# Performance work log

Measured on AMD Instinct MI355X. Metric: run time of the kernel, lower is better.

## Reference

```python
import jax, jax.numpy as jnp
import numpy as np

N = 8192      # total QM atoms (concatenated over batch)
L = 6         # num_interactions / trajectory length
F = 256       # hidden_size
FH = F // 2
D_RBF = 32    # distance_embedding_size
E = 131072    # total probe edges
P = 32768     # total probes
CUTOFF = 4.0


def silu(x):
    return x * jax.nn.sigmoid(x)


def setup_inputs() -> dict:
    key = jax.random.key(0)
    ks = jax.random.split(key, 20)
    g = lambda k, shp, s=1.0: jax.random.normal(k, shp, dtype=jnp.float32) * s
    s_stack = g(ks[0], (N, L, F))
    v_stack = g(ks[1], (N, L, 3, F))
    # positions in a 2A box so all probe-atom distances < cutoff=4A
    atom_xyz = jax.random.uniform(ks[2], (N, 3), dtype=jnp.float32) * 2.0
    probe_xyz = jax.random.uniform(ks[3], (P, 3), dtype=jnp.float32) * 2.0
    cell = jnp.eye(3, dtype=jnp.float32) * 2.0
    probe_edges_displacement = jnp.zeros((E, 3), dtype=jnp.float32)
    atom_idx = jax.random.randint(ks[4], (E,), 0, N)
    probe_idx = jax.random.randint(ks[5], (E,), 0, P)
    probe_edges = jnp.stack([atom_idx, probe_idx], axis=1)
    in_dim = D_RBF + 3 * F  # e_pi || q_pi || n_i || S_JK
    return {
        's_stack': s_stack,
        'v_stack': v_stack,
        'atom_xyz': atom_xyz,
        'probe_xyz': probe_xyz,
        'cell': cell,
        'probe_edges_displacement': probe_edges_displacement,
        # JK attention MLP: F -> F/2 -> 1
        'attn_w1': g(ks[6], (F, FH), 1.0 / np.sqrt(F)),
        'attn_b1': jnp.zeros((FH,), jnp.float32),
        'attn_w2': g(ks[7], (FH, 1), 1.0 / np.sqrt(FH)),
        'attn_b2': jnp.zeros((1,), jnp.float32),
        # readout msg MLP: (D_rbf+3F) -> F -> F/2 -> 1
        'msg_w1': g(ks[8], (in_dim, F), 1.0 / np.sqrt(in_dim)),
        'msg_b1': jnp.zeros((F,), jnp.float32),
        'msg_w2': g(ks[9], (F, FH), 1.0 / np.sqrt(F)),
        'msg_b2': jnp.zeros((FH,), jnp.float32),
        'msg_w3': g(ks[10], (FH, 1), 1.0 / np.sqrt(FH)),
        'msg_b3': jnp.zeros((1,), jnp.float32),
        'probe_edges': probe_edges,
    }


def reference(s_stack, v_stack, atom_xyz, probe_xyz, cell, probe_edges_displacement,
              attn_w1, attn_b1, attn_w2, attn_b2,
              msg_w1, msg_b1, msg_w2, msg_b2, msg_w3, msg_b3,
              probe_edges):
    # ---- JKNetAggregation: node-level attention over layer trajectory ----
    h = silu(jnp.einsum('nlf,fh->nlh', s_stack, attn_w1) + attn_b1)   # [N,L,F/2]
    logits = (jnp.einsum('nlh,ho->nlo', h, attn_w2) + attn_b2)[..., 0]  # [N,L]
    a = jax.nn.softmax(logits, axis=1)                                  # [N,L]
    S_JK = jnp.einsum('nl,nlf->nf', a, s_stack)                         # [N,F]
    V_JK = jnp.einsum('nl,nlcf->ncf', a, v_stack)                       # [N,3,F]

    # ---- InfoBottleneckReadout: gather -> per-edge MLP -> scatter ----
    atom_idx = probe_edges[:, 0]
    probe_idx = probe_edges[:, 1]
    shift = probe_edges_displacement @ cell                             # [E,3] PBC shift
    diff = probe_xyz[probe_idx] - (atom_xyz[atom_idx] + shift)          # [E,3]
    dist = jnp.linalg.norm(diff, axis=-1)                               # [E]
    d = dist[:, None]
    n = jnp.arange(1, D_RBF + 1, dtype=jnp.float32)
    e_pi = jnp.sin(d * n * jnp.pi / CUTOFF) / (d + 1e-8)                # [E,D_rbf] sinc RBF
    r_hat = diff / (d + 1e-8)                                           # [E,3]
    V_e = V_JK[atom_idx]                                                # [E,3,F]
    q_pi = jnp.einsum('ecf,ec->ef', V_e, r_hat)                         # [E,F]
    n_i = jnp.linalg.norm(V_JK, axis=1)                                 # [N,F]
    h_pi = jnp.concatenate([e_pi, q_pi, n_i[atom_idx], S_JK[atom_idx]], axis=-1)  # [E,D_rbf+3F]
    m = silu(h_pi @ msg_w1 + msg_b1)
    m = silu(m @ msg_w2 + msg_b2)
    m = (m @ msg_w3 + msg_b3)[:, 0]                                     # [E]
    cw = jnp.where(dist < CUTOFF, 0.5 * (jnp.cos(jnp.pi * dist / CUTOFF) + 1.0), 0.0)
    rho = jax.ops.segment_sum(m * cw, probe_idx, num_segments=P)        # [P]
    return rho
```

## Files before the change

### kernel.cpp

```cpp
#include <hip/hip_runtime.h>
#include <math.h>
#include <stdint.h>


#define L_DIM 6
#define F_DIM 256
#define FH_DIM 128
#define DRBF 32
#define CUTOFF_F 4.0f
#define PI_F 3.14159265358979323846f

using bf16x8 = __attribute__((ext_vector_type(8))) short;
using f32x4v = __attribute__((ext_vector_type(4))) float;

__device__ __forceinline__ float silu_f(float x){ return x / (1.f + __expf(-x)); }

__device__ __forceinline__ unsigned short f2bf(float f){
    uint32_t u = __float_as_uint(f);
    uint32_t r = (u + 0x7fffu + ((u >> 16) & 1u)) >> 16;
    return (unsigned short)r;
}

__global__ __launch_bounds__(256) void kPrep(
    const float* __restrict__ msg_w1, const float* __restrict__ msg_w2,
    const float* __restrict__ attn_w1,
    unsigned short* __restrict__ w1bt, unsigned short* __restrict__ w1cdt,
    unsigned short* __restrict__ w2t, unsigned short* __restrict__ wA1t,
    float* __restrict__ rho, int P, int* __restrict__ cntpos, int CN)
{
    int idx = blockIdx.x * 256 + threadIdx.x;
    if (idx < 65536){
        int k = idx >> 8, j = idx & 255;
        w1bt[(size_t)j * 256 + k] = f2bf(msg_w1[(size_t)(DRBF + k) * F_DIM + j]);
    } else if (idx < 196608){
        int i2 = idx - 65536;
        int k = i2 >> 8, j = i2 & 255;
        w1cdt[(size_t)j * 512 + k] = f2bf(msg_w1[(size_t)(DRBF + 256 + k) * F_DIM + j]);
    } else if (idx < 229376){
        int i3 = idx - 196608;
        int k = i3 >> 7, h = i3 & 127;
        w2t[(size_t)h * 256 + k] = f2bf(msg_w2[(size_t)k * FH_DIM + h]);
    } else if (idx < 262144){
        int i4 = idx - 229376;
        int j = i4 >> 8, k = i4 & 255;
        wA1t[(size_t)j * 256 + k] = f2bf(attn_w1[(size_t)k * FH_DIM + j]);
    } else if (idx < 262144 + 32768){
        int i5 = idx - 262144;
        if (i5 < P) rho[i5] = 0.f;
    } else {
        int i6 = idx - 262144 - 32768;
        if (i6 < CN) cntpos[i6] = 0;
    }
}

__global__ __launch_bounds__(256) void kAW(
    const float* __restrict__ s_stack, const float* __restrict__ v_stack,
    const unsigned short* __restrict__ wA1t,
    const float* __restrict__ attn_b1, const float* __restrict__ attn_w2,
    unsigned short* __restrict__ VJKb, unsigned short* __restrict__ NISb, int N)
{
    __shared__ float part[4][48];
    __shared__ float aw_l[8][8];

    const int t  = threadIdx.x;
    const int l  = t & 63;
    const int w  = t >> 6;
    const int lm = l & 15, lq = l >> 4;

    bf16x8 bfr[2][8];
    #pragma unroll
    for (int nt2 = 0; nt2 < 2; nt2++){
        const int col = w*32 + nt2*16 + lm;
        #pragma unroll
        for (int kb = 0; kb < 8; kb++)
            bfr[nt2][kb] = *(const bf16x8*)(wA1t + (size_t)col * 256 + kb*32 + lq*8);
    }
    const float b1a = attn_b1[w*32 + lm];
    const float b1b = attn_b1[w*32 + 16 + lm];
    const float w2a = attn_w2[w*32 + lm];
    const float w2b = attn_w2[w*32 + 16 + lm];

    const int n0 = blockIdx.x * 8;
    const size_t rbase = (size_t)n0 * L_DIM;
    const size_t rmax  = (size_t)N * L_DIM - 1;

    #pragma unroll
    for (int mt = 0; mt < 3; mt++){
        const size_t r0 = rbase + mt * 16;
        bf16x8 af[8];
        #pragma unroll
        for (int kb = 0; kb < 8; kb++){
            size_t row = r0 + lm; if (row > rmax) row = rmax;
            const float* ap = s_stack + row * 256 + kb*32 + lq*8;
            float4 fa = *(const float4*)ap;
            float4 fb = *(const float4*)(ap + 4);
            bf16x8 v;
            v[0] = (short)f2bf(fa.x); v[1] = (short)f2bf(fa.y);
            v[2] = (short)f2bf(fa.z); v[3] = (short)f2bf(fa.w);
            v[4] = (short)f2bf(fb.x); v[5] = (short)f2bf(fb.y);
            v[6] = (short)f2bf(fb.z); v[7] = (short)f2bf(fb.w);
            af[kb] = v;
        }
        f32x4v a0 = {0.f,0.f,0.f,0.f}, a1 = {0.f,0.f,0.f,0.f};
        #pragma unroll
        for (int kb = 0; kb < 8; kb++){
            a0 = __builtin_amdgcn_mfma_f32_16x16x32_bf16(af[kb], bfr[0][kb], a0, 0, 0, 0);
            a1 = __builtin_amdgcn_mfma_f32_16x16x32_bf16(af[kb], bfr[1][kb], a1, 0, 0, 0);
        }
        #pragma unroll
        for (int r = 0; r < 4; r++){
            float p = silu_f(a0[r] + b1a) * w2a + silu_f(a1[r] + b1b) * w2b;
            #pragma unroll
            for (int m = 8; m >= 1; m >>= 1) p += __shfl_xor(p, m, 64);
            if (lm == 0) part[w][mt*16 + lq*4 + r] = p;
        }
    }
    __syncthreads();
    if (t < 48) part[0][t] = part[0][t] + part[1][t] + part[2][t] + part[3][t];
    __syncthreads();
    if (t < 8){
        float e[L_DIM]; float mx = -1e30f;
        #pragma unroll
        for (int l6 = 0; l6 < L_DIM; l6++) mx = fmaxf(mx, part[0][t*L_DIM + l6]);
        float s = 0.f;
        #pragma unroll
        for (int l6 = 0; l6 < L_DIM; l6++){ e[l6] = __expf(part[0][t*L_DIM + l6] - mx); s += e[l6]; }
        float inv = 1.f / s;
        #pragma unroll
        for (int l6 = 0; l6 < L_DIM; l6++) aw_l[t][l6] = e[l6] * inv;
    }
    __syncthreads();

    #pragma unroll
    for (int aa = 0; aa < 2; aa++){
        const int n = min(n0 + w*2 + aa, N - 1);
        float aw[L_DIM];
        #pragma unroll
        for (int l6 = 0; l6 < L_DIM; l6++) aw[l6] = aw_l[w*2 + aa][l6];

        const float* sp = s_stack + (size_t)n * (L_DIM * F_DIM) + l * 4;
        const float* vp = v_stack + (size_t)n * (L_DIM * 3 * F_DIM) + l * 4;
        float4 v0 = {0.f,0.f,0.f,0.f}, v1 = {0.f,0.f,0.f,0.f}, v2 = {0.f,0.f,0.f,0.f};
        float4 sj = {0.f,0.f,0.f,0.f};
        #pragma unroll
        for (int l6 = 0; l6 < L_DIM; l6++){
            const float a = aw[l6];
            float4 ss = *(const float4*)(sp + (size_t)l6 * F_DIM);
            float4 x0 = *(const float4*)(vp + (size_t)(l6*3+0) * F_DIM);
            float4 x1 = *(const float4*)(vp + (size_t)(l6*3+1) * F_DIM);
            float4 x2 = *(const float4*)(vp + (size_t)(l6*3+2) * F_DIM);
            v0.x = fmaf(a, x0.x, v0.x); v0.y = fmaf(a, x0.y, v0.y);
            v0.z = fmaf(a, x0.z, v0.z); v0.w = fmaf(a, x0.w, v0.w);
            v1.x = fmaf(a, x1.x, v1.x); v1.y = fmaf(a, x1.y, v1.y);
            v1.z = fmaf(a, x1.z, v1.z); v1.w = fmaf(a, x1.w, v1.w);
            v2.x = fmaf(a, x2.x, v2.x); v2.y = fmaf(a, x2.y, v2.y);
            v2.z = fmaf(a, x2.z, v2.z); v2.w = fmaf(a, x2.w, v2.w);
            sj.x = fmaf(a, ss.x, sj.x); sj.y = fmaf(a, ss.y, sj.y);
            sj.z = fmaf(a, ss.z, sj.z); sj.w = fmaf(a, ss.w, sj.w);
        }
        float4 ni;
        ni.x = sqrtf(v0.x*v0.x + v1.x*v1.x + v2.x*v2.x);
        ni.y = sqrtf(v0.y*v0.y + v1.y*v1.y + v2.y*v2.y);
        ni.z = sqrtf(v0.z*v0.z + v1.z*v1.z + v2.z*v2.z);
        ni.w = sqrtf(v0.w*v0.w + v1.w*v1.w + v2.w*v2.w);

        ushort4 o;
        o = (ushort4){f2bf(v0.x), f2bf(v0.y), f2bf(v0.z), f2bf(v0.w)};
        *(ushort4*)&VJKb[((size_t)n*3 + 0) * F_DIM + l*4] = o;
        o = (ushort4){f2bf(v1.x), f2bf(v1.y), f2bf(v1.z), f2bf(v1.w)};
        *(ushort4*)&VJKb[((size_t)n*3 + 1) * F_DIM + l*4] = o;
        o = (ushort4){f2bf(v2.x), f2bf(v2.y), f2bf(v2.z), f2bf(v2.w)};
        *(ushort4*)&VJKb[((size_t)n*3 + 2) * F_DIM + l*4] = o;
        o = (ushort4){f2bf(ni.x), f2bf(ni.y), f2bf(ni.z), f2bf(ni.w)};
        *(ushort4*)&NISb[(size_t)n * 512 + l*4] = o;
        o = (ushort4){f2bf(sj.x), f2bf(sj.y), f2bf(sj.z), f2bf(sj.w)};
        *(ushort4*)&NISb[(size_t)n * 512 + 256 + l*4] = o;
    }
}

__global__ __launch_bounds__(256) void kA2(
    const unsigned short* __restrict__ VJKb, const unsigned short* __restrict__ w1bt,
    const unsigned short* __restrict__ NISb, const unsigned short* __restrict__ w1cdt,
    const float* __restrict__ msg_b1,
    float* __restrict__ UT4, int gU)
{
    const int t  = threadIdx.x;
    const int l  = t & 63;
    const int w  = t >> 6;
    const int lm = l & 15, lq = l >> 4;

    if ((int)blockIdx.x < gU){
        bf16x8 bfr[4][8];
        #pragma unroll
        for (int ct = 0; ct < 4; ct++)
            #pragma unroll
            for (int kb = 0; kb < 8; kb++)
                bfr[ct][kb] = *(const bf16x8*)(w1bt + (size_t)(w*64 + ct*16 + lm) * 256 + kb*32 + lq*8);

        const int r00 = blockIdx.x * 128;
        #pragma unroll 1
        for (int mt = 0; mt < 8; mt++){
            const int r0 = r00 + mt * 16;
            bf16x8 af[8];
            #pragma unroll
            for (int kb = 0; kb < 8; kb++)
                af[kb] = *(const bf16x8*)(VJKb + (size_t)(r0 + lm) * 256 + kb*32 + lq*8);
            f32x4v acc[4];
            #pragma unroll
            for (int ct = 0; ct < 4; ct++) acc[ct] = (f32x4v){0.f,0.f,0.f,0.f};
            #pragma unroll
            for (int kb = 0; kb < 8; kb++)
                #pragma unroll
                for (int ct = 0; ct < 4; ct++)
                    acc[ct] = __builtin_amdgcn_mfma_f32_16x16x32_bf16(af[kb], bfr[ct][kb], acc[ct], 0, 0, 0);
            #pragma unroll
            for (int ct = 0; ct < 4; ct++){
                const int col = w*64 + ct*16 + lm;
                #pragma unroll
                for (int r = 0; r < 4; r++){
                    const int row = r0 + lq*4 + r;
                    const int n = row / 3, c = row - n*3;
                    UT4[(((size_t)n << 8) + col) * 4 + c] = acc[ct][r];
                }
            }
        }
    } else {
        const int bid = blockIdx.x - gU;
        const int ch = bid & 1;
        const int bm = bid >> 1;

        bf16x8 bfr[2][16];
        #pragma unroll
        for (int ct = 0; ct < 2; ct++)
            #pragma unroll
            for (int kb = 0; kb < 16; kb++)
                bfr[ct][kb] = *(const bf16x8*)(w1cdt + (size_t)(ch*128 + w*32 + ct*16 + lm) * 512 + kb*32 + lq*8);

        const int r00 = bm * 128;
        #pragma unroll 1
        for (int mt = 0; mt < 8; mt++){
            const int r0 = r00 + mt * 16;
            bf16x8 af[16];
            #pragma unroll
            for (int kb = 0; kb < 16; kb++)
                af[kb] = *(const bf16x8*)(NISb + (size_t)(r0 + lm) * 512 + kb*32 + lq*8);
            f32x4v acc[2];
            #pragma unroll
            for (int ct = 0; ct < 2; ct++) acc[ct] = (f32x4v){0.f,0.f,0.f,0.f};
            #pragma unroll
            for (int kb = 0; kb < 16; kb++)
                #pragma unroll
                for (int ct = 0; ct < 2; ct++)
                    acc[ct] = __builtin_amdgcn_mfma_f32_16x16x32_bf16(af[kb], bfr[ct][kb], acc[ct], 0, 0, 0);
            #pragma unroll
            for (int ct = 0; ct < 2; ct++){
                const int col = ch*128 + w*32 + ct*16 + lm;
                const float bias = msg_b1[col];
                #pragma unroll
                for (int r = 0; r < 4; r++){
                    const int n = r0 + lq*4 + r;
                    UT4[(((size_t)n << 8) + col) * 4 + 3] = acc[ct][r] + bias;
                }
            }
        }
    }
}

__global__ __launch_bounds__(256) void kHist(const int* __restrict__ pe, int* __restrict__ cnt, int E){
    int e = blockIdx.x * 256 + threadIdx.x;
    if (e < E) atomicAdd(&cnt[pe[(size_t)e*2]], 1);
}

__global__ __launch_bounds__(1024) void kScan(const int* __restrict__ cnt, int* __restrict__ off, int N){
    __shared__ int sums[1024];
    const int t = threadIdx.x;
    const int base = t * 8;
    int c[8]; int s = 0;
    #pragma unroll
    for (int j = 0; j < 8; j++){
        int v = (base + j < N) ? cnt[base + j] : 0;
        c[j] = s; s += v;
    }
    sums[t] = s;
    __syncthreads();
    for (int d = 1; d < 1024; d <<= 1){
        int v = (t >= d) ? sums[t - d] : 0;
        __syncthreads();
        sums[t] += v;
        __syncthreads();
    }
    int excl = (t == 0) ? 0 : sums[t - 1];
    #pragma unroll
    for (int j = 0; j < 8; j++)
        if (base + j < N) off[base + j] = excl + c[j];
    if (t == 1023) off[N] = sums[1023];
}

__global__ __launch_bounds__(256) void kScatter(const int* __restrict__ pe,
    const int* __restrict__ off, int* __restrict__ pos, int* __restrict__ perm, int E){
    int e = blockIdx.x * 256 + threadIdx.x;
    if (e < E){
        int i = pe[(size_t)e*2];
        int slot = atomicAdd(&pos[i], 1);
        perm[off[i] + slot] = e;
    }
}

__global__ __launch_bounds__(256) void kB1(
    const int* __restrict__ pe, const float* __restrict__ disp,
    const float* __restrict__ cell,
    const float* __restrict__ atom_xyz, const float* __restrict__ probe_xyz,
    const float* __restrict__ UT4,
    const float* __restrict__ msg_w1,
    const unsigned short* __restrict__ w2t, const float* __restrict__ msg_b2,
    const float* __restrict__ msg_w3, const float* __restrict__ msg_b3,
    const int* __restrict__ perm,
    float* __restrict__ rho, int E)
{
    __shared__ unsigned short x_lds[32 * 256];
    __shared__ unsigned short epi_b[32 * 40];
    __shared__ int   ai_l[32];
    __shared__ int   pp_l[32];
    __shared__ float4 rc4_l[32];
    __shared__ float part[4][32];

    char* xbase = (char*)x_lds;

    const int t  = threadIdx.x;
    const int l  = t & 63;
    const int w  = t >> 6;
    const int lq = l >> 4;
    const int lm = l & 15;

    const float c0 = cell[0], c1 = cell[1], c2 = cell[2];
    const float c3 = cell[3], c4 = cell[4], c5 = cell[5];
    const float c6 = cell[6], c7 = cell[7], c8 = cell[8];

    bf16x8 w1afr[4];
    #pragma unroll
    for (int nt = 0; nt < 4; nt++){
        const int col = w*64 + nt*16 + lm;
        bf16x8 v;
        #pragma unroll
        for (int j = 0; j < 8; j++)
            v[j] = (short)f2bf(msg_w1[(size_t)(lq*8 + j) * F_DIM + col]);
        w1afr[nt] = v;
    }

    bf16x8 bfr[2][8];
    #pragma unroll
    for (int nt2 = 0; nt2 < 2; nt2++){
        const int h = w*32 + nt2*16 + lm;
        #pragma unroll
        for (int kb = 0; kb < 8; kb++)
            bfr[nt2][kb] = *(const bf16x8*)(w2t + (size_t)h * F_DIM + kb*32 + lq*8);
    }
    const float b2v0 = msg_b2[w*32 + lm];
    const float b2v1 = msg_b2[w*32 + 16 + lm];
    const float w3v0 = msg_w3[w*32 + lm];
    const float w3v1 = msg_w3[w*32 + 16 + lm];
    const float b3   = msg_b3[0];

    const int e0 = blockIdx.x * 128;

    int ee_r[4], ia_r[4], ip_r[4];
    #pragma unroll
    for (int bb = 0; bb < 4; bb++){
        int s = min(e0 + bb*32 + (t >> 3), E - 1);
        ee_r[bb] = perm[s];
    }
    #pragma unroll
    for (int bb = 0; bb < 4; bb++){
        ia_r[bb] = pe[(size_t)ee_r[bb]*2];
        ip_r[bb] = pe[(size_t)ee_r[bb]*2 + 1];
    }

    #pragma unroll 1
    for (int bb = 0; bb < 4; bb++){
        const int e0b = e0 + bb * 32;

        {
            const int slot = t >> 3, q = t & 7;
            const int ee = ee_r[bb];
            const int ia = ia_r[bb];
            const int ip = ip_r[bb];
            const float d0 = disp[(size_t)ee*3], d1 = disp[(size_t)ee*3+1], d2 = disp[(size_t)ee*3+2];
            const float sx = d0*c0 + d1*c3 + d2*c6;
            const float sy = d0*c1 + d1*c4 + d2*c7;
            const float sz = d0*c2 + d1*c5 + d2*c8;
            const float dx = probe_xyz[(size_t)ip*3+0] - (atom_xyz[(size_t)ia*3+0] + sx);
            const float dy = probe_xyz[(size_t)ip*3+1] - (atom_xyz[(size_t)ia*3+1] + sy);
            const float dz = probe_xyz[(size_t)ip*3+2] - (atom_xyz[(size_t)ia*3+2] + sz);
            const float dist = sqrtf(dx*dx + dy*dy + dz*dz);
            const float inv  = 1.f / (dist + 1e-8f);
            const float base = dist * (PI_F / CUTOFF_F);
            ushort4 eb;
            eb.x = f2bf(__sinf(base * (float)(q*4 + 1)) * inv);
            eb.y = f2bf(__sinf(base * (float)(q*4 + 2)) * inv);
            eb.z = f2bf(__sinf(base * (float)(q*4 + 3)) * inv);
            eb.w = f2bf(__sinf(base * (float)(q*4 + 4)) * inv);
            *(ushort4*)&epi_b[slot*40 + q*4] = eb;
            if (q == 0){
                ai_l[slot] = ia;
                pp_l[slot] = ip;
                float cw = (dist < CUTOFF_F) ? 0.5f * (__cosf(base) + 1.f) : 0.f;
                rc4_l[slot] = (float4){dx*inv, dy*inv, dz*inv, cw};
            }
        }
        __syncthreads();

        f32x4v pacc[2][4];
        #pragma unroll
        for (int mt = 0; mt < 2; mt++)
            #pragma unroll
            for (int nt = 0; nt < 4; nt++) pacc[mt][nt] = (f32x4v){0.f,0.f,0.f,0.f};
        #pragma unroll
        for (int mt = 0; mt < 2; mt++){
            const bf16x8 af = *(const bf16x8*)&epi_b[(mt*16 + lm)*40 + lq*8];
            #pragma unroll
            for (int nt = 0; nt < 4; nt++)
                pacc[mt][nt] = __builtin_amdgcn_mfma_f32_16x16x32_bf16(af, w1afr[nt], pacc[mt][nt], 0, 0, 0);
        }

        #pragma unroll
        for (int mt = 0; mt < 2; mt++){
            #pragma unroll
            for (int r = 0; r < 4; r++){
                const int e = mt*16 + lq*4 + r;
                const int i = ai_l[e];
                const float4 rc = rc4_l[e];
                const float* up = UT4 + ((size_t)i << 10);
                #pragma unroll
                for (int nt = 0; nt < 4; nt++){
                    const int col = w*64 + nt*16 + lm;
                    const float4 ut = *(const float4*)(up + (size_t)col * 4);
                    float z = pacc[mt][nt][r] + ut.w;
                    z = fmaf(rc.x, ut.x, fmaf(rc.y, ut.y, fmaf(rc.z, ut.z, z)));
                    const int wofs = e*512 + ((col*2) ^ ((e & 7) << 4));
                    *(unsigned short*)(xbase + wofs) = f2bf(silu_f(z));
                }
            }
        }
        __syncthreads();

        f32x4v acc00 = {0.f,0.f,0.f,0.f}, acc01 = {0.f,0.f,0.f,0.f};
        f32x4v acc10 = {0.f,0.f,0.f,0.f}, acc11 = {0.f,0.f,0.f,0.f};
        const int eA0 = lm;
        const int eA1 = 16 + lm;
        #pragma unroll
        for (int kb = 0; kb < 8; kb++){
            const int ko = kb*64 + lq*16;
            bf16x8 af0 = *(const bf16x8*)(xbase + eA0*512 + (ko ^ ((eA0 & 7) << 4)));
            bf16x8 af1 = *(const bf16x8*)(xbase + eA1*512 + (ko ^ ((eA1 & 7) << 4)));
            acc00 = __builtin_amdgcn_mfma_f32_16x16x32_bf16(af0, bfr[0][kb], acc00, 0, 0, 0);
            acc01 = __builtin_amdgcn_mfma_f32_16x16x32_bf16(af0, bfr[1][kb], acc01, 0, 0, 0);
            acc10 = __builtin_amdgcn_mfma_f32_16x16x32_bf16(af1, bfr[0][kb], acc10, 0, 0, 0);
            acc11 = __builtin_amdgcn_mfma_f32_16x16x32_bf16(af1, bfr[1][kb], acc11, 0, 0, 0);
        }

        float pr0[4], pr1[4];
        #pragma unroll
        for (int r = 0; r < 4; r++){
            pr0[r] = silu_f(acc00[r] + b2v0) * w3v0 + silu_f(acc01[r] + b2v1) * w3v1;
            pr1[r] = silu_f(acc10[r] + b2v0) * w3v0 + silu_f(acc11[r] + b2v1) * w3v1;
        }
        #pragma unroll
        for (int r = 0; r < 4; r++){
            #pragma unroll
            for (int m = 8; m >= 1; m >>= 1){
                pr0[r] += __shfl_xor(pr0[r], m, 64);
                pr1[r] += __shfl_xor(pr1[r], m, 64);
            }
        }
        if (lm == 0){
            #pragma unroll
            for (int r = 0; r < 4; r++){
                part[w][lq*4 + r]      = pr0[r];
                part[w][16 + lq*4 + r] = pr1[r];
            }
        }
        __syncthreads();

        if (t < 32 && (e0b + t) < E){
            float tot = part[0][t] + part[1][t] + part[2][t] + part[3][t] + b3;
            atomicAdd(&rho[pp_l[t]], tot * rc4_l[t].w);
        }
        __syncthreads();
    }
}

extern "C" void kernel_launch(void* const* d_in, const int* in_sizes, int n_in,
                              void* d_out, int out_size, void* d_ws, size_t ws_size,
                              hipStream_t stream)
{
    const float* s_stack   = (const float*)d_in[0];
    const float* v_stack   = (const float*)d_in[1];
    const float* atom_xyz  = (const float*)d_in[2];
    const float* probe_xyz = (const float*)d_in[3];
    const float* cell      = (const float*)d_in[4];
    const float* disp      = (const float*)d_in[5];
    const float* attn_w1   = (const float*)d_in[6];
    const float* attn_b1   = (const float*)d_in[7];
    const float* attn_w2   = (const float*)d_in[8];
    const float* msg_w1    = (const float*)d_in[10];
    const float* msg_b1    = (const float*)d_in[11];
    const float* msg_w2    = (const float*)d_in[12];
    const float* msg_b2    = (const float*)d_in[13];
    const float* msg_w3    = (const float*)d_in[14];
    const float* msg_b3    = (const float*)d_in[15];
    const int*   pe        = (const int*)d_in[16];

    const int N = in_sizes[0] / (L_DIM * F_DIM);
    const int E = in_sizes[16] / 2;
    const int P = out_size;
    const size_t NF = (size_t)N * F_DIM;

    float* ws = (float*)d_ws;
    unsigned short* VJKb = (unsigned short*)ws;
    unsigned short* NISb = VJKb + 3*NF;
    float* UT4 = ws + (5*NF)/2;
    unsigned short* w1bt  = (unsigned short*)(ws + (13*NF)/2);
    unsigned short* w1cdt = w1bt + 65536;
    unsigned short* w2t   = w1cdt + 131072;
    unsigned short* wA1t  = w2t + 32768;
    int* cnt  = (int*)(wA1t + 32768);
    int* pos  = cnt + N;
    int* offs = pos + N;
    int* perm = offs + N + 1;

    const int prepElems = 262144 + 32768 + 2 * N;
    kPrep<<<(prepElems + 255) / 256, 256, 0, stream>>>(
        msg_w1, msg_w2, attn_w1, w1bt, w1cdt, w2t, wA1t,
        (float*)d_out, P, cnt, 2 * N);

    kAW<<<(N + 7) / 8, 256, 0, stream>>>(s_stack, v_stack, wA1t, attn_b1, attn_w2,
                                         VJKb, NISb, N);

    const int gU = (3 * N) / 128;
    const int gT = (N / 128) * 2;
    kA2<<<gU + gT, 256, 0, stream>>>(VJKb, w1bt, NISb, w1cdt, msg_b1, UT4, gU);

    const int gE = (E + 255) / 256;
    kHist<<<gE, 256, 0, stream>>>(pe, cnt, E);
    kScan<<<1, 1024, 0, stream>>>(cnt, offs, N);
    kScatter<<<gE, 256, 0, stream>>>(pe, offs, pos, perm, E);

    kB1<<<(E + 127) / 128, 256, 0, stream>>>(pe, disp, cell, atom_xyz, probe_xyz,
                                             UT4, msg_w1,
                                             w2t, msg_b2, msg_w3, msg_b3,
                                             perm, (float*)d_out, E);
}
```

Before: 186.8 us.

## Fuse histogram and scatter into existing kernels and lower kB1 register pressure

The edge histogram moves into kAW's tail, where each block counts 128 edges, and the scatter into extra blocks of kA2. This drops two kernel launches and lets the index sort overlap with the dense GEMM work. In kB1, the second-layer weight fragments are no longer held in registers but loaded per k-step from global or L2. The first-layer accumulators are scoped per m-tile and launch bounds ask for 6 waves per SIMD to raise occupancy, at the cost of repeated weight loads.

Result: slower. 312.9 us (+67.5%).

```diff
diff --git a/kernel.cpp b/kernel.cpp
--- a/kernel.cpp
+++ b/kernel.cpp
@@ -57,7 +57,8 @@
     const float* __restrict__ s_stack, const float* __restrict__ v_stack,
     const unsigned short* __restrict__ wA1t,
     const float* __restrict__ attn_b1, const float* __restrict__ attn_w2,
-    unsigned short* __restrict__ VJKb, unsigned short* __restrict__ NISb, int N)
+    unsigned short* __restrict__ VJKb, unsigned short* __restrict__ NISb,
+    const int* __restrict__ pe, int* __restrict__ cnt, int E, int N)
 {
     __shared__ float part[4][48];
     __shared__ float aw_l[8][8];
@@ -176,18 +177,35 @@
         o = (ushort4){f2bf(sj.x), f2bf(sj.y), f2bf(sj.z), f2bf(sj.w)};
         *(ushort4*)&NISb[(size_t)n * 512 + 256 + l*4] = o;
     }
+
+    {
+        int e = blockIdx.x * 128 + t;
+        if (t < 128 && e < E) atomicAdd(&cnt[pe[(size_t)e*2]], 1);
+    }
 }
 
 __global__ __launch_bounds__(256) void kA2(
     const unsigned short* __restrict__ VJKb, const unsigned short* __restrict__ w1bt,
     const unsigned short* __restrict__ NISb, const unsigned short* __restrict__ w1cdt,
-    const float* __restrict__ msg_b1,
-    float* __restrict__ UT4, int gU)
+    const float* __restrict__ msg_b1, float* __restrict__ UT4,
+    const int* __restrict__ pe, const int* __restrict__ offs,
+    int* __restrict__ pos, int* __restrict__ perm, int E,
+    int gU, int gUT)
 {
     const int t  = threadIdx.x;
     const int l  = t & 63;
     const int w  = t >> 6;
     const int lm = l & 15, lq = l >> 4;
+
+    if ((int)blockIdx.x >= gUT){
+        int e = (blockIdx.x - gUT) * 256 + t;
+        if (e < E){
+            int i = pe[(size_t)e*2];
+            int slot = atomicAdd(&pos[i], 1);
+            perm[offs[i] + slot] = e;
+        }
+        return;
+    }
 
     if ((int)blockIdx.x < gU){
         bf16x8 bfr[4][8];
@@ -266,11 +284,6 @@
     }
 }
 
-__global__ __launch_bounds__(256) void kHist(const int* __restrict__ pe, int* __restrict__ cnt, int E){
-    int e = blockIdx.x * 256 + threadIdx.x;
-    if (e < E) atomicAdd(&cnt[pe[(size_t)e*2]], 1);
-}
-
 __global__ __launch_bounds__(1024) void kScan(const int* __restrict__ cnt, int* __restrict__ off, int N){
     __shared__ int sums[1024];
     const int t = threadIdx.x;
@@ -296,17 +309,7 @@
     if (t == 1023) off[N] = sums[1023];
 }
 
-__global__ __launch_bounds__(256) void kScatter(const int* __restrict__ pe,
-    const int* __restrict__ off, int* __restrict__ pos, int* __restrict__ perm, int E){
-    int e = blockIdx.x * 256 + threadIdx.x;
-    if (e < E){
-        int i = pe[(size_t)e*2];
-        int slot = atomicAdd(&pos[i], 1);
-        perm[off[i] + slot] = e;
-    }
-}
-
-__global__ __launch_bounds__(256) void kB1(
+__global__ __launch_bounds__(256, 6) void kB1(
     const int* __restrict__ pe, const float* __restrict__ disp,
     const float* __restrict__ cell,
     const float* __restrict__ atom_xyz, const float* __restrict__ probe_xyz,
@@ -347,19 +350,14 @@
         w1afr[nt] = v;
     }
 
-    bf16x8 bfr[2][8];
-    #pragma unroll
-    for (int nt2 = 0; nt2 < 2; nt2++){
-        const int h = w*32 + nt2*16 + lm;
-        #pragma unroll
-        for (int kb = 0; kb < 8; kb++)
-            bfr[nt2][kb] = *(const bf16x8*)(w2t + (size_t)h * F_DIM + kb*32 + lq*8);
-    }
     const float b2v0 = msg_b2[w*32 + lm];
     const float b2v1 = msg_b2[w*32 + 16 + lm];
     const float w3v0 = msg_w3[w*32 + lm];
     const float w3v1 = msg_w3[w*32 + 16 + lm];
     const float b3   = msg_b3[0];
+
+    const unsigned short* w2p0 = w2t + (size_t)(w*32 + lm)      * F_DIM + lq*8;
+    const unsigned short* w2p1 = w2t + (size_t)(w*32 + 16 + lm) * F_DIM + lq*8;
 
     const int e0 = blockIdx.x * 128;
 
@@ -409,21 +407,16 @@
         }
         __syncthreads();
 
-        f32x4v pacc[2][4];
-        #pragma unroll
-        for (int mt = 0; mt < 2; mt++)
-            #pragma unroll
-            for (int nt = 0; nt < 4; nt++) pacc[mt][nt] = (f32x4v){0.f,0.f,0.f,0.f};
         #pragma unroll
         for (int mt = 0; mt < 2; mt++){
+            f32x4v pacc[4];
+            #pragma unroll
+            for (int nt = 0; nt < 4; nt++) pacc[nt] = (f32x4v){0.f,0.f,0.f,0.f};
             const bf16x8 af = *(const bf16x8*)&epi_b[(mt*16 + lm)*40 + lq*8];
             #pragma unroll
             for (int nt = 0; nt < 4; nt++)
-                pacc[mt][nt] = __builtin_amdgcn_mfma_f32_16x16x32_bf16(af, w1afr[nt], pacc[mt][nt], 0, 0, 0);
-        }
-
-        #pragma unroll
-        for (int mt = 0; mt < 2; mt++){
+                pacc[nt] = __builtin_amdgcn_mfma_f32_16x16x32_bf16(af, w1afr[nt], pacc[nt], 0, 0, 0);
+
             #pragma unroll
             for (int r = 0; r < 4; r++){
                 const int e = mt*16 + lq*4 + r;
@@ -434,7 +427,7 @@
                 for (int nt = 0; nt < 4; nt++){
                     const int col = w*64 + nt*16 + lm;
                     const float4 ut = *(const float4*)(up + (size_t)col * 4);
-                    float z = pacc[mt][nt][r] + ut.w;
+                    float z = pacc[nt][r] + ut.w;
                     z = fmaf(rc.x, ut.x, fmaf(rc.y, ut.y, fmaf(rc.z, ut.z, z)));
                     const int wofs = e*512 + ((col*2) ^ ((e & 7) << 4));
                     *(unsigned short*)(xbase + wofs) = f2bf(silu_f(z));
@@ -450,12 +443,14 @@
         #pragma unroll
         for (int kb = 0; kb < 8; kb++){
             const int ko = kb*64 + lq*16;
+            bf16x8 b0 = *(const bf16x8*)(w2p0 + kb*32);
+            bf16x8 b1 = *(const bf16x8*)(w2p1 + kb*32);
             bf16x8 af0 = *(const bf16x8*)(xbase + eA0*512 + (ko ^ ((eA0 & 7) << 4)));
             bf16x8 af1 = *(const bf16x8*)(xbase + eA1*512 + (ko ^ ((eA1 & 7) << 4)));
-            acc00 = __builtin_amdgcn_mfma_f32_16x16x32_bf16(af0, bfr[0][kb], acc00, 0, 0, 0);
-            acc01 = __builtin_amdgcn_mfma_f32_16x16x32_bf16(af0, bfr[1][kb], acc01, 0, 0, 0);
-            acc10 = __builtin_amdgcn_mfma_f32_16x16x32_bf16(af1, bfr[0][kb], acc10, 0, 0, 0);
-            acc11 = __builtin_amdgcn_mfma_f32_16x16x32_bf16(af1, bfr[1][kb], acc11, 0, 0, 0);
+            acc00 = __builtin_amdgcn_mfma_f32_16x16x32_bf16(af0, b0, acc00, 0, 0, 0);
+            acc01 = __builtin_amdgcn_mfma_f32_16x16x32_bf16(af0, b1, acc01, 0, 0, 0);
+            acc10 = __builtin_amdgcn_mfma_f32_16x16x32_bf16(af1, b0, acc10, 0, 0, 0);
+            acc11 = __builtin_amdgcn_mfma_f32_16x16x32_bf16(af1, b1, acc11, 0, 0, 0);
         }
 
         float pr0[4], pr1[4];
@@ -534,16 +529,16 @@
         (float*)d_out, P, cnt, 2 * N);
 
     kAW<<<(N + 7) / 8, 256, 0, stream>>>(s_stack, v_stack, wA1t, attn_b1, attn_w2,
-                                         VJKb, NISb, N);
-
-    const int gU = (3 * N) / 128;
-    const int gT = (N / 128) * 2;
-    kA2<<<gU + gT, 256, 0, stream>>>(VJKb, w1bt, NISb, w1cdt, msg_b1, UT4, gU);
-
-    const int gE = (E + 255) / 256;
-    kHist<<<gE, 256, 0, stream>>>(pe, cnt, E);
+                                         VJKb, NISb, pe, cnt, E, N);
+
     kScan<<<1, 1024, 0, stream>>>(cnt, offs, N);
-    kScatter<<<gE, 256, 0, stream>>>(pe, offs, pos, perm, E);
+
+    const int gU  = (3 * N) / 128;
+    const int gT  = (N / 128) * 2;
+    const int gUT = gU + gT;
+    const int gS  = (E + 255) / 256;
+    kA2<<<gUT + gS, 256, 0, stream>>>(VJKb, w1bt, NISb, w1cdt, msg_b1, UT4,
+                                      pe, offs, pos, perm, E, gU, gUT);
 
     kB1<<<(E + 127) / 128, 256, 0, stream>>>(pe, disp, cell, atom_xyz, probe_xyz,
                                              UT4, msg_w1,
```
